# Optimization experiments

Hardware: AMD Instinct MI355X
Metric: run time of the kernel (lower is better)

Reference implementation:

```python
import jax, jax.numpy as jnp
import numpy as np

N_NODES = 100000
FEAT = 128
N_EDGES = 1600000


def setup_inputs() -> dict:
    key = jax.random.key(0)
    k1, k2, k3, k4, k5 = jax.random.split(key, 5)
    weight = jax.random.normal(k1, (N_NODES, FEAT), dtype=jnp.float32)
    cj = jax.random.uniform(k2, (N_NODES, 1), dtype=jnp.float32)
    ci = jax.random.uniform(k3, (N_NODES, 1), dtype=jnp.float32)
    src = jax.random.randint(k4, (N_EDGES,), 0, N_NODES, dtype=jnp.int32)
    dst = jax.random.randint(k5, (N_EDGES,), 0, N_NODES, dtype=jnp.int32)
    return {"weight": weight, "cj": cj, "ci": ci, "src": src, "dst": dst}


def reference(weight, cj, ci, src, dst):
    # feat = weight * dropout(cj); dropout_rate=0.0 -> identity
    feat = weight * cj                      # [N, F]
    msgs = feat[src]                        # [E, F] copy_src gather
    h = jax.ops.segment_sum(msgs, dst, num_segments=weight.shape[0])  # [N, F]
    return h * ci                           # dst-side normalize
```

## Files before the change

### kernel.cpp

```cpp
#include <hip/hip_runtime.h>
#include <hip/hip_bf16.h>

#define FEAT 128
#define BINW 128
#define BINSHIFT 7
#define MAXBIN 1024
#define MAXTILE 1024
#define FS_CAP 4096

__device__ __forceinline__ unsigned short f2b(float f) {
    __hip_bfloat16 h = __float2bfloat16(f);
    return *reinterpret_cast<unsigned short*>(&h);
}
__device__ __forceinline__ float b2f_lo(unsigned u) {
    unsigned x = u << 16;
    float f;
    __builtin_memcpy(&f, &x, 4);
    return f;
}
__device__ __forceinline__ float b2f_hi(unsigned u) {
    unsigned x = u & 0xFFFF0000u;
    float f;
    __builtin_memcpy(&f, &x, 4);
    return f;
}
__device__ __forceinline__ unsigned int pack2(float lo, float hi) {
    return (unsigned int)f2b(lo) | ((unsigned int)f2b(hi) << 16);
}


__global__ void convert_hist_bins_kernel(const float* __restrict__ weight,
                                         const float* __restrict__ cj,
                                         const int* __restrict__ dst,
                                         unsigned short* __restrict__ feat16,
                                         int* __restrict__ cnt,
                                         int N, int E, int NBIN, int tb, int ipt) {
    __shared__ int h[MAXBIN];
    int tile = blockIdx.x;
    for (int b = threadIdx.x; b < NBIN; b += 256) h[b] = 0;
    __syncthreads();

    int NC = N * (FEAT / 8);
    int cbase = tile * 256 * ipt;
    for (int j = 0; j < ipt; ++j) {
        int i = cbase + j * 256 + threadIdx.x;
        if (i < NC) {
            int row = i >> 4;
            int seg = i & 15;
            float c = cj[row];
            const float4* p = reinterpret_cast<const float4*>(
                weight + (size_t)row * FEAT + seg * 8);
            float4 a = p[0], b4 = p[1];
            uint4 o;
            o.x = pack2(a.x * c, a.y * c);
            o.y = pack2(a.z * c, a.w * c);
            o.z = pack2(b4.x * c, b4.y * c);
            o.w = pack2(b4.z * c, b4.w * c);
            *reinterpret_cast<uint4*>(feat16 + (size_t)i * 8) = o;
        }
    }

    int e0 = tile * tb;
    int iters = tb >> 8;
    for (int i = 0; i < iters; ++i) {
        int e = e0 + i * 256 + threadIdx.x;
        if (e < E) atomicAdd(&h[dst[e] >> BINSHIFT], 1);
    }
    __syncthreads();
    for (int b = threadIdx.x; b < NBIN; b += 256) cnt[(size_t)tile * NBIN + b] = h[b];
}

__global__ void bin_scan_kernel(const int* __restrict__ cnt, int* __restrict__ base_local,
                                int* __restrict__ binTot, int NBIN, int NTILE) {
    __shared__ int s[MAXTILE];
    int b = blockIdx.x;
    int t = threadIdx.x;
    int v = (t < NTILE) ? cnt[(size_t)t * NBIN + b] : 0;
    s[t] = v;
    __syncthreads();
    for (int off = 1; off < MAXTILE; off <<= 1) {
        int u = (t >= off) ? s[t - off] : 0;
        __syncthreads();
        s[t] += u;
        __syncthreads();
    }
    if (t < NTILE) base_local[(size_t)t * NBIN + b] = s[t] - v;
    if (t == MAXTILE - 1) binTot[b] = s[t];
}

__global__ void scan_tot_kernel(const int* __restrict__ binTot, int* __restrict__ binStart,
                                int NBIN) {
    __shared__ int s[1024];
    int t = threadIdx.x;
    int v = (t < NBIN) ? binTot[t] : 0;
    s[t] = v;
    __syncthreads();
    for (int off = 1; off < 1024; off <<= 1) {
        int u = (t >= off) ? s[t - off] : 0;
        __syncthreads();
        s[t] += u;
        __syncthreads();
    }
    if (t < NBIN) binStart[t] = s[t] - v;
    if (t == NBIN - 1) binStart[NBIN] = s[t];
}

__global__ void scatter_pairs_kernel(const int* __restrict__ src, const int* __restrict__ dst,
                                     const int* __restrict__ base_local,
                                     const int* __restrict__ binStart,
                                     unsigned* __restrict__ pair,
                                     int E, int NBIN, int tb) {
    __shared__ int base_l[MAXBIN];
    __shared__ int cur[MAXBIN];
    int tile = blockIdx.x;
    for (int b = threadIdx.x; b < NBIN; b += 256) {
        base_l[b] = binStart[b] + base_local[(size_t)tile * NBIN + b];
        cur[b] = 0;
    }
    __syncthreads();
    int e0 = tile * tb;
    int iters = tb >> 8;
    for (int i = 0; i < iters; ++i) {
        int e = e0 + i * 256 + threadIdx.x;
        if (e < E) {
            int d = dst[e];
            int b = d >> BINSHIFT;
            int pos = atomicAdd(&cur[b], 1);
            pair[base_l[b] + pos] = (unsigned)src[e] | ((unsigned)(d & (BINW - 1)) << 17);
        }
    }
}

__global__ void fine_sort_kernel(unsigned* __restrict__ pair,
                                 unsigned* __restrict__ tmp,
                                 const int* __restrict__ binStart,
                                 int* __restrict__ offsets,
                                 int N, int E) {
    __shared__ int cnt[BINW];
    __shared__ int sbase[BINW];
    __shared__ unsigned stage[FS_CAP];
    int bin = blockIdx.x;
    int t = threadIdx.x;
    if (t < BINW) cnt[t] = 0;
    __syncthreads();
    int start = binStart[bin];
    int end   = binStart[bin + 1];
    bool lds_ok = (end - start) <= FS_CAP;

    if (lds_ok) {
        for (int k = start + t; k < end; k += 256) {
            unsigned p = pair[k];
            stage[k - start] = p;
            atomicAdd(&cnt[p >> 17], 1);
        }
    } else {
        for (int k = start + t; k < end; k += 256) {
            unsigned p = pair[k];
            tmp[k] = p;
            atomicAdd(&cnt[p >> 17], 1);
        }
    }
    __syncthreads();
    int mine = (t < BINW) ? cnt[t] : 0;
    if (t < BINW) sbase[t] = mine;
    __syncthreads();
    for (int d = 1; d < BINW; d <<= 1) {
        int v = 0;
        if (t < BINW && t >= d) v = sbase[t - d];
        __syncthreads();
        if (t < BINW) sbase[t] += v;
        __syncthreads();
    }
    if (t < BINW) {
        int excl = sbase[t] - mine;
        int node = (bin << BINSHIFT) + t;
        if (node < N) offsets[node] = start + excl;
        sbase[t] = start + excl;
        cnt[t] = 0;
    }
    if (bin == 0 && t == 0) offsets[N] = E;
    __syncthreads();
    if (lds_ok) {
        for (int k = start + t; k < end; k += 256) {
            unsigned p = stage[k - start];
            int ld = p >> 17;
            int pos = atomicAdd(&cnt[ld], 1);
            pair[sbase[ld] + pos] = p & 0x1FFFF;
        }
    } else {
        for (int k = start + t; k < end; k += 256) {
            unsigned p = tmp[k];
            int ld = p >> 17;
            int pos = atomicAdd(&cnt[ld], 1);
            pair[sbase[ld] + pos] = p & 0x1FFFF;
        }
    }
}

__global__ void gather_kernel(const unsigned short* __restrict__ feat16,
                              const float* __restrict__ ci,
                              const int* __restrict__ offsets,
                              const int* __restrict__ src_sorted,
                              float* __restrict__ out, int N) {
    int gt = blockIdx.x * blockDim.x + threadIdx.x;
    int node = gt >> 6;
    if (node >= N) return;
    int lane = gt & 63;
    int fi   = (lane & 15) << 3;
    int q    = lane >> 4;
    int start = offsets[node];
    int end   = offsets[node + 1];
    float acc[8] = {0.f, 0.f, 0.f, 0.f, 0.f, 0.f, 0.f, 0.f};
    #pragma unroll 4
    for (int k = start + q; k < end; k += 4) {
        int s = src_sorted[k];
        uint4 u = *reinterpret_cast<const uint4*>(feat16 + ((size_t)s << 7) + fi);
        acc[0] += b2f_lo(u.x); acc[1] += b2f_hi(u.x);
        acc[2] += b2f_lo(u.y); acc[3] += b2f_hi(u.y);
        acc[4] += b2f_lo(u.z); acc[5] += b2f_hi(u.z);
        acc[6] += b2f_lo(u.w); acc[7] += b2f_hi(u.w);
    }
    #pragma unroll
    for (int j = 0; j < 8; ++j) {
        acc[j] += __shfl_xor(acc[j], 16);
        acc[j] += __shfl_xor(acc[j], 32);
    }
    if (q == 0) {
        float c = ci[node];
        float4 v0 = make_float4(acc[0] * c, acc[1] * c, acc[2] * c, acc[3] * c);
        float4 v1 = make_float4(acc[4] * c, acc[5] * c, acc[6] * c, acc[7] * c);
        float* o = out + ((size_t)node << 7) + fi;
        *reinterpret_cast<float4*>(o)     = v0;
        *reinterpret_cast<float4*>(o + 4) = v1;
    }
}


__global__ void zero_ints_kernel(int* __restrict__ p, int n) {
    int i = blockIdx.x * blockDim.x + threadIdx.x;
    if (i < n) p[i] = 0;
}

__global__ void convert_hist_kernel(const float* __restrict__ weight,
                                    const float* __restrict__ cj,
                                    const int* __restrict__ dst,
                                    int* __restrict__ counts,
                                    unsigned short* __restrict__ feat16,
                                    int N, int E) {
    int i = blockIdx.x * blockDim.x + threadIdx.x;
    int NC = N * (FEAT / 8);
    if (i < NC) {
        int row = i >> 4;
        int seg = i & 15;
        float c = cj[row];
        const float4* p = reinterpret_cast<const float4*>(weight + (size_t)row * FEAT + seg * 8);
        float4 a = p[0], b = p[1];
        uint4 o;
        o.x = pack2(a.x * c, a.y * c);
        o.y = pack2(a.z * c, a.w * c);
        o.z = pack2(b.x * c, b.y * c);
        o.w = pack2(b.z * c, b.w * c);
        *reinterpret_cast<uint4*>(feat16 + (size_t)i * 8) = o;
    }
    if (i < E) atomicAdd(&counts[dst[i]], 1);
}

__global__ void block_sum_kernel(const int* __restrict__ counts, int* __restrict__ bsum, int N) {
    __shared__ int s[256];
    int i = blockIdx.x * 256 + threadIdx.x;
    s[threadIdx.x] = (i < N) ? counts[i] : 0;
    __syncthreads();
    for (int off = 128; off > 0; off >>= 1) {
        if (threadIdx.x < off) s[threadIdx.x] += s[threadIdx.x + off];
        __syncthreads();
    }
    if (threadIdx.x == 0) bsum[blockIdx.x] = s[0];
}

__global__ void scan_bsum_kernel(int* __restrict__ bsum, int nb) {
    __shared__ int s[512];
    int t = threadIdx.x;
    int mine = (t < nb) ? bsum[t] : 0;
    s[t] = mine;
    __syncthreads();
    for (int off = 1; off < 512; off <<= 1) {
        int v = (t >= off) ? s[t - off] : 0;
        __syncthreads();
        s[t] += v;
        __syncthreads();
    }
    if (t < nb) bsum[t] = s[t] - mine;
}

__global__ void scan_counts_kernel(const int* __restrict__ counts, const int* __restrict__ bsum,
                                   int* __restrict__ offsets, int* __restrict__ cursor,
                                   int N, int E) {
    __shared__ int s[256];
    int t = threadIdx.x;
    int i = blockIdx.x * 256 + t;
    int mine = (i < N) ? counts[i] : 0;
    s[t] = mine;
    __syncthreads();
    for (int off = 1; off < 256; off <<= 1) {
        int v = (t >= off) ? s[t - off] : 0;
        __syncthreads();
        s[t] += v;
        __syncthreads();
    }
    if (i < N) {
        int o = bsum[blockIdx.x] + s[t] - mine;
        offsets[i] = o;
        cursor[i] = o;
    }
    if (i == 0 && blockIdx.x == 0) offsets[N] = E;
}

__global__ void bucket_kernel(const int* __restrict__ src, const int* __restrict__ dst,
                              int* __restrict__ cursor,
                              int* __restrict__ src_sorted, int E) {
    int i = blockIdx.x * blockDim.x + threadIdx.x;
    if (i < E) {
        int pos = atomicAdd(&cursor[dst[i]], 1);
        src_sorted[pos] = src[i];
    }
}


__global__ void gcmc_zero_kernel(float4* __restrict__ out, int n4) {
    int i = blockIdx.x * blockDim.x + threadIdx.x;
    if (i < n4) out[i] = make_float4(0.f, 0.f, 0.f, 0.f);
}

__global__ void gcmc_scatter_kernel(const float* __restrict__ weight,
                                    const float* __restrict__ cj,
                                    const int* __restrict__ src,
                                    const int* __restrict__ dst,
                                    float* __restrict__ out,
                                    int n_edges) {
    int t = blockIdx.x * blockDim.x + threadIdx.x;
    int e = t >> 5;
    int f = (t & 31) << 2;
    if (e >= n_edges) return;
    int s = src[e];
    int d = dst[e];
    float c = cj[s];
    const float4 w = *reinterpret_cast<const float4*>(weight + (size_t)s * FEAT + f);
    float* o = out + (size_t)d * FEAT + f;
    unsafeAtomicAdd(o + 0, w.x * c);
    unsafeAtomicAdd(o + 1, w.y * c);
    unsafeAtomicAdd(o + 2, w.z * c);
    unsafeAtomicAdd(o + 3, w.w * c);
}

__global__ void gcmc_scale_kernel(float4* __restrict__ out,
                                  const float* __restrict__ ci, int n4) {
    int i = blockIdx.x * blockDim.x + threadIdx.x;
    if (i < n4) {
        float c = ci[i >> 5];
        float4 v = out[i];
        v.x *= c; v.y *= c; v.z *= c; v.w *= c;
        out[i] = v;
    }
}


static inline size_t align256(size_t x) { return (x + 255) & ~(size_t)255; }

extern "C" void kernel_launch(void* const* d_in, const int* in_sizes, int n_in,
                              void* d_out, int out_size, void* d_ws, size_t ws_size,
                              hipStream_t stream) {
    const float* weight = (const float*)d_in[0];
    const float* cj     = (const float*)d_in[1];
    const float* ci     = (const float*)d_in[2];
    const int*   src    = (const int*)d_in[3];
    const int*   dst    = (const int*)d_in[4];
    float* out = (float*)d_out;

    const int N = in_sizes[1];
    const int E = in_sizes[3];

    const int NBIN = (N + BINW - 1) >> BINSHIFT;

    for (int tb = 2048; tb <= 8192; tb *= 4) {
        const int NTILE = (E + tb - 1) / tb;
        if (NTILE > MAXTILE) continue;

        size_t o_feat = 0;
        size_t o_pair = align256(o_feat + (size_t)N * FEAT * 2);
        size_t o_cnt  = align256(o_pair + (size_t)E * 4);
        size_t o_base = align256(o_cnt + (size_t)NTILE * NBIN * 4);
        size_t o_tot  = align256(o_base + (size_t)NTILE * NBIN * 4);
        size_t o_bs   = align256(o_tot + (size_t)NBIN * 4);
        size_t o_off  = align256(o_bs + (size_t)(NBIN + 1) * 4);
        size_t need   = o_off + (size_t)(N + 1) * 4;

        if (ws_size < need || NBIN > MAXBIN || N > (1 << 17) || out_size < E) continue;

        char* ws = (char*)d_ws;
        unsigned short* feat16 = (unsigned short*)(ws + o_feat);
        unsigned* pair   = (unsigned*)(ws + o_pair);
        int* cnt         = (int*)(ws + o_cnt);
        int* base_local  = (int*)(ws + o_base);
        int* binTot      = (int*)(ws + o_tot);
        int* binStart    = (int*)(ws + o_bs);
        int* offsets     = (int*)(ws + o_off);

        const int NC  = N * (FEAT / 8);
        const int ipt = (NC + NTILE * 256 - 1) / (NTILE * 256);

        convert_hist_bins_kernel<<<NTILE, 256, 0, stream>>>(
            weight, cj, dst, feat16, cnt, N, E, NBIN, tb, ipt);
        bin_scan_kernel<<<NBIN, MAXTILE, 0, stream>>>(cnt, base_local, binTot, NBIN, NTILE);
        scan_tot_kernel<<<1, 1024, 0, stream>>>(binTot, binStart, NBIN);
        scatter_pairs_kernel<<<NTILE, 256, 0, stream>>>(src, dst, base_local, binStart,
                                                        pair, E, NBIN, tb);
        fine_sort_kernel<<<NBIN, 256, 0, stream>>>(pair, (unsigned*)out, binStart,
                                                   offsets, N, E);
        long threads = (long)N * 64;
        gather_kernel<<<(int)((threads + 255) / 256), 256, 0, stream>>>(
            feat16, ci, offsets, (const int*)pair, out, N);
        return;
    }

    const int NB = (N + 255) / 256;
    size_t m_off = 0;
    size_t m_cur = align256(m_off + (size_t)(N + 1) * 4);
    size_t m_bsm = align256(m_cur + (size_t)N * 4);
    size_t m_src = align256(m_bsm + 512 * 4);
    size_t m_ft  = align256(m_src + (size_t)E * 4);
    size_t need_mid = m_ft + (size_t)N * FEAT * 2;

    if (ws_size >= need_mid && NB <= 512) {
        char* ws = (char*)d_ws;
        int* offsets    = (int*)(ws + m_off);
        int* cursor     = (int*)(ws + m_cur);
        int* bsum       = (int*)(ws + m_bsm);
        int* src_sorted = (int*)(ws + m_src);
        unsigned short* feat16 = (unsigned short*)(ws + m_ft);

        zero_ints_kernel<<<NB, 256, 0, stream>>>(cursor, N);
        {
            long T = (long)N * (FEAT / 8);
            if ((long)E > T) T = E;
            convert_hist_kernel<<<(int)((T + 255) / 256), 256, 0, stream>>>(
                weight, cj, dst, cursor, feat16, N, E);
        }
        block_sum_kernel<<<NB, 256, 0, stream>>>(cursor, bsum, N);
        scan_bsum_kernel<<<1, 512, 0, stream>>>(bsum, NB);
        scan_counts_kernel<<<NB, 256, 0, stream>>>(cursor, bsum, offsets, cursor, N, E);
        bucket_kernel<<<(E + 255) / 256, 256, 0, stream>>>(src, dst, cursor, src_sorted, E);
        long threads = (long)N * 64;
        gather_kernel<<<(int)((threads + 255) / 256), 256, 0, stream>>>(
            feat16, ci, offsets, src_sorted, out, N);
        return;
    }

    const int total = N * FEAT;
    const int n4 = total >> 2;
    gcmc_zero_kernel<<<(n4 + 255) / 256, 256, 0, stream>>>((float4*)out, n4);
    const long threads = (long)E * 32;
    gcmc_scatter_kernel<<<(int)((threads + 255) / 256), 256, 0, stream>>>(
        weight, cj, src, dst, out, E);
    gcmc_scale_kernel<<<(n4 + 255) / 256, 256, 0, stream>>>((float4*)out, ci, n4);
}
```

Measured before the change: 131.4 us.

## Fuse fine sort into gather and assign bin starts atomically

Merges the per-bin fine sort with the gather so each block sorts its bin's edges in LDS and aggregates features directly, so sorted edges and offsets no longer round-trip through global memory. The bin-total scan kernel is dropped: bin starts come from an atomic cursor instead of a prefix scan. Bins shrink to 64 nodes, tile count is capped at 256, and the convert grid is doubled so conversion is spread across more blocks. Bins larger than the LDS capacity are handled by chunking, with read-modify-write of the output; the atomic ordering makes bin layout nondeterministic and the gather now runs with fewer, larger blocks.

After: 143.6 us. 9.3% more time.

```diff
diff --git a/kernel.cpp b/kernel.cpp
--- a/kernel.cpp
+++ b/kernel.cpp
@@ -2,11 +2,11 @@
 #include <hip/hip_bf16.h>
 
 #define FEAT 128
-#define BINW 128
-#define BINSHIFT 7
-#define MAXBIN 1024
-#define MAXTILE 1024
-#define FS_CAP 4096
+#define BINW 64
+#define BINSHIFT 6
+#define MAXBIN 2048
+#define MAXTILE 256
+#define FS_CAP 2048
 
 __device__ __forceinline__ unsigned short f2b(float f) {
     __hip_bfloat16 h = __float2bfloat16(f);
@@ -34,11 +34,12 @@
                                          const int* __restrict__ dst,
                                          unsigned short* __restrict__ feat16,
                                          int* __restrict__ cnt,
-                                         int N, int E, int NBIN, int tb, int ipt) {
+                                         int* __restrict__ cursor,
+                                         int N, int E, int NBIN, int NTILE,
+                                         int tb, int ipt) {
     __shared__ int h[MAXBIN];
     int tile = blockIdx.x;
-    for (int b = threadIdx.x; b < NBIN; b += 256) h[b] = 0;
-    __syncthreads();
+    if (tile == 0 && threadIdx.x == 0) *cursor = 0;
 
     int NC = N * (FEAT / 8);
     int cbase = tile * 256 * ipt;
@@ -60,18 +61,27 @@
         }
     }
 
-    int e0 = tile * tb;
-    int iters = tb >> 8;
-    for (int i = 0; i < iters; ++i) {
-        int e = e0 + i * 256 + threadIdx.x;
-        if (e < E) atomicAdd(&h[dst[e] >> BINSHIFT], 1);
-    }
-    __syncthreads();
-    for (int b = threadIdx.x; b < NBIN; b += 256) cnt[(size_t)tile * NBIN + b] = h[b];
-}
-
-__global__ void bin_scan_kernel(const int* __restrict__ cnt, int* __restrict__ base_local,
-                                int* __restrict__ binTot, int NBIN, int NTILE) {
+    if (tile < NTILE) {
+        for (int b = threadIdx.x; b < NBIN; b += 256) h[b] = 0;
+        __syncthreads();
+        int e0 = tile * tb;
+        int iters = tb >> 8;
+        for (int i = 0; i < iters; ++i) {
+            int e = e0 + i * 256 + threadIdx.x;
+            if (e < E) atomicAdd(&h[dst[e] >> BINSHIFT], 1);
+        }
+        __syncthreads();
+        for (int b = threadIdx.x; b < NBIN; b += 256)
+            cnt[(size_t)tile * NBIN + b] = h[b];
+    }
+}
+
+__global__ void bin_scan_kernel(const int* __restrict__ cnt,
+                                int* __restrict__ base_local,
+                                int* __restrict__ binStart,
+                                int* __restrict__ binLen,
+                                int* __restrict__ cursor,
+                                int NBIN, int NTILE) {
     __shared__ int s[MAXTILE];
     int b = blockIdx.x;
     int t = threadIdx.x;
@@ -85,24 +95,11 @@
         __syncthreads();
     }
     if (t < NTILE) base_local[(size_t)t * NBIN + b] = s[t] - v;
-    if (t == MAXTILE - 1) binTot[b] = s[t];
-}
-
-__global__ void scan_tot_kernel(const int* __restrict__ binTot, int* __restrict__ binStart,
-                                int NBIN) {
-    __shared__ int s[1024];
-    int t = threadIdx.x;
-    int v = (t < NBIN) ? binTot[t] : 0;
-    s[t] = v;
-    __syncthreads();
-    for (int off = 1; off < 1024; off <<= 1) {
-        int u = (t >= off) ? s[t - off] : 0;
-        __syncthreads();
-        s[t] += u;
-        __syncthreads();
-    }
-    if (t < NBIN) binStart[t] = s[t] - v;
-    if (t == NBIN - 1) binStart[NBIN] = s[t];
+    if (t == MAXTILE - 1) {
+        int tot = s[t];
+        binLen[b] = tot;
+        binStart[b] = atomicAdd(cursor, tot);
+    }
 }
 
 __global__ void scatter_pairs_kernel(const int* __restrict__ src, const int* __restrict__ dst,
@@ -131,69 +128,198 @@
     }
 }
 
-__global__ void fine_sort_kernel(unsigned* __restrict__ pair,
-                                 unsigned* __restrict__ tmp,
-                                 const int* __restrict__ binStart,
-                                 int* __restrict__ offsets,
-                                 int N, int E) {
+__global__ void __launch_bounds__(512)
+gather_sort_kernel(const unsigned short* __restrict__ feat16,
+                   const float* __restrict__ ci,
+                   const int* __restrict__ binStart,
+                   const int* __restrict__ binLen,
+                   const unsigned* __restrict__ pair,
+                   float* __restrict__ out, int N) {
+    __shared__ unsigned stage[FS_CAP];
+    __shared__ int srt[FS_CAP];
     __shared__ int cnt[BINW];
     __shared__ int sbase[BINW];
-    __shared__ unsigned stage[FS_CAP];
+
     int bin = blockIdx.x;
     int t = threadIdx.x;
-    if (t < BINW) cnt[t] = 0;
-    __syncthreads();
     int start = binStart[bin];
-    int end   = binStart[bin + 1];
-    bool lds_ok = (end - start) <= FS_CAP;
-
-    if (lds_ok) {
-        for (int k = start + t; k < end; k += 256) {
-            unsigned p = pair[k];
-            stage[k - start] = p;
+    int len   = binLen[bin];
+    int w    = t >> 6;
+    int lane = t & 63;
+    int q    = lane >> 4;
+    int fi   = (lane & 15) << 3;
+
+    int nchunks = (len + FS_CAP - 1) / FS_CAP;
+    if (nchunks < 1) nchunks = 1;
+
+    for (int ic = 0; ic < nchunks; ++ic) {
+        __syncthreads();
+        int cs = start + ic * FS_CAP;
+        int clen = len - ic * FS_CAP;
+        if (clen > FS_CAP) clen = FS_CAP;
+        if (clen < 0) clen = 0;
+
+        if (t < BINW) cnt[t] = 0;
+        __syncthreads();
+        for (int k = t; k < clen; k += 512) {
+            unsigned p = pair[cs + k];
+            stage[k] = p;
             atomicAdd(&cnt[p >> 17], 1);
         }
-    } else {
-        for (int k = start + t; k < end; k += 256) {
-            unsigned p = pair[k];
-            tmp[k] = p;
-            atomicAdd(&cnt[p >> 17], 1);
-        }
-    }
-    __syncthreads();
-    int mine = (t < BINW) ? cnt[t] : 0;
-    if (t < BINW) sbase[t] = mine;
-    __syncthreads();
-    for (int d = 1; d < BINW; d <<= 1) {
-        int v = 0;
-        if (t < BINW && t >= d) v = sbase[t - d];
-        __syncthreads();
-        if (t < BINW) sbase[t] += v;
-        __syncthreads();
-    }
-    if (t < BINW) {
-        int excl = sbase[t] - mine;
-        int node = (bin << BINSHIFT) + t;
-        if (node < N) offsets[node] = start + excl;
-        sbase[t] = start + excl;
-        cnt[t] = 0;
-    }
-    if (bin == 0 && t == 0) offsets[N] = E;
-    __syncthreads();
-    if (lds_ok) {
-        for (int k = start + t; k < end; k += 256) {
-            unsigned p = stage[k - start];
+        __syncthreads();
+        int mine = (t < BINW) ? cnt[t] : 0;
+        if (t < BINW) sbase[t] = mine;
+        __syncthreads();
+        for (int d = 1; d < BINW; d <<= 1) {
+            int v = 0;
+            if (t < BINW && t >= d) v = sbase[t - d];
+            __syncthreads();
+            if (t < BINW) sbase[t] += v;
+            __syncthreads();
+        }
+        if (t < BINW) { sbase[t] -= mine; cnt[t] = 0; }
+        __syncthreads();
+        for (int k = t; k < clen; k += 512) {
+            unsigned p = stage[k];
             int ld = p >> 17;
             int pos = atomicAdd(&cnt[ld], 1);
-            pair[sbase[ld] + pos] = p & 0x1FFFF;
-        }
-    } else {
-        for (int k = start + t; k < end; k += 256) {
-            unsigned p = tmp[k];
-            int ld = p >> 17;
-            int pos = atomicAdd(&cnt[ld], 1);
-            pair[sbase[ld] + pos] = p & 0x1FFFF;
-        }
+            srt[sbase[ld] + pos] = (int)(p & 0x1FFFF);
+        }
+        __syncthreads();
+
+        bool first = (ic == 0);
+        bool last  = (ic == nchunks - 1);
+        for (int j = 0; j < 8; ++j) {
+            int ln = (w << 3) + j;
+            int node = (bin << BINSHIFT) + ln;
+            if (node >= N) break;
+            int sb = sbase[ln];
+            int c  = cnt[ln];
+            float acc[8] = {0.f, 0.f, 0.f, 0.f, 0.f, 0.f, 0.f, 0.f};
+            #pragma unroll 4
+            for (int k = q; k < c; k += 4) {
+                int s = srt[sb + k];
+                uint4 u = *reinterpret_cast<const uint4*>(
+                    feat16 + ((size_t)s << 7) + fi);
+                acc[0] += b2f_lo(u.x); acc[1] += b2f_hi(u.x);
+                acc[2] += b2f_lo(u.y); acc[3] += b2f_hi(u.y);
+                acc[4] += b2f_lo(u.z); acc[5] += b2f_hi(u.z);
+                acc[6] += b2f_lo(u.w); acc[7] += b2f_hi(u.w);
+            }
+            #pragma unroll
+            for (int r = 0; r < 8; ++r) {
+                acc[r] += __shfl_xor(acc[r], 16);
+                acc[r] += __shfl_xor(acc[r], 32);
+            }
+            if (q == 0) {
+                float* o = out + ((size_t)node << 7) + fi;
+                float4 v0 = make_float4(acc[0], acc[1], acc[2], acc[3]);
+                float4 v1 = make_float4(acc[4], acc[5], acc[6], acc[7]);
+                if (!first) {
+                    float4 p0 = *reinterpret_cast<float4*>(o);
+                    float4 p1 = *reinterpret_cast<float4*>(o + 4);
+                    v0.x += p0.x; v0.y += p0.y; v0.z += p0.z; v0.w += p0.w;
+                    v1.x += p1.x; v1.y += p1.y; v1.z += p1.z; v1.w += p1.w;
+                }
+                if (last) {
+                    float cc = ci[node];
+                    v0.x *= cc; v0.y *= cc; v0.z *= cc; v0.w *= cc;
+                    v1.x *= cc; v1.y *= cc; v1.z *= cc; v1.w *= cc;
+                }
+                *reinterpret_cast<float4*>(o)     = v0;
+                *reinterpret_cast<float4*>(o + 4) = v1;
+            }
+        }
+    }
+}
+
+
+__global__ void zero_ints_kernel(int* __restrict__ p, int n) {
+    int i = blockIdx.x * blockDim.x + threadIdx.x;
+    if (i < n) p[i] = 0;
+}
+
+__global__ void convert_hist_kernel(const float* __restrict__ weight,
+                                    const float* __restrict__ cj,
+                                    const int* __restrict__ dst,
+                                    int* __restrict__ counts,
+                                    unsigned short* __restrict__ feat16,
+                                    int N, int E) {
+    int i = blockIdx.x * blockDim.x + threadIdx.x;
+    int NC = N * (FEAT / 8);
+    if (i < NC) {
+        int row = i >> 4;
+        int seg = i & 15;
+        float c = cj[row];
+        const float4* p = reinterpret_cast<const float4*>(weight + (size_t)row * FEAT + seg * 8);
+        float4 a = p[0], b = p[1];
+        uint4 o;
+        o.x = pack2(a.x * c, a.y * c);
+        o.y = pack2(a.z * c, a.w * c);
+        o.z = pack2(b.x * c, b.y * c);
+        o.w = pack2(b.z * c, b.w * c);
+        *reinterpret_cast<uint4*>(feat16 + (size_t)i * 8) = o;
+    }
+    if (i < E) atomicAdd(&counts[dst[i]], 1);
+}
+
+__global__ void block_sum_kernel(const int* __restrict__ counts, int* __restrict__ bsum, int N) {
+    __shared__ int s[256];
+    int i = blockIdx.x * 256 + threadIdx.x;
+    s[threadIdx.x] = (i < N) ? counts[i] : 0;
+    __syncthreads();
+    for (int off = 128; off > 0; off >>= 1) {
+        if (threadIdx.x < off) s[threadIdx.x] += s[threadIdx.x + off];
+        __syncthreads();
+    }
+    if (threadIdx.x == 0) bsum[blockIdx.x] = s[0];
+}
+
+__global__ void scan_bsum_kernel(int* __restrict__ bsum, int nb) {
+    __shared__ int s[512];
+    int t = threadIdx.x;
+    int mine = (t < nb) ? bsum[t] : 0;
+    s[t] = mine;
+    __syncthreads();
+    for (int off = 1; off < 512; off <<= 1) {
+        int v = (t >= off) ? s[t - off] : 0;
+        __syncthreads();
+        s[t] += v;
+        __syncthreads();
+    }
+    if (t < nb) bsum[t] = s[t] - mine;
+}
+
+__global__ void scan_counts_kernel(const int* __restrict__ counts, const int* __restrict__ bsum,
+                                   int* __restrict__ offsets, int* __restrict__ cursor,
+                                   int N, int E) {
+    __shared__ int s[256];
+    int t = threadIdx.x;
+    int i = blockIdx.x * 256 + t;
+    int mine = (i < N) ? counts[i] : 0;
+    s[t] = mine;
+    __syncthreads();
+    for (int off = 1; off < 256; off <<= 1) {
+        int v = (t >= off) ? s[t - off] : 0;
+        __syncthreads();
+        s[t] += v;
+        __syncthreads();
+    }
+    if (i < N) {
+        int o = bsum[blockIdx.x] + s[t] - mine;
+        offsets[i] = o;
+        cursor[i] = o;
+    }
+    if (i == 0 && blockIdx.x == 0) offsets[N] = E;
+}
+
+__global__ void bucket_kernel(const int* __restrict__ src, const int* __restrict__ dst,
+                              int* __restrict__ cursor,
+                              int* __restrict__ src_sorted, int E) {
+    int i = blockIdx.x * blockDim.x + threadIdx.x;
+    if (i < E) {
+        int pos = atomicAdd(&cursor[dst[i]], 1);
+        src_sorted[pos] = src[i];
     }
 }
 
@@ -236,96 +362,6 @@
 }
 
 
-__global__ void zero_ints_kernel(int* __restrict__ p, int n) {
-    int i = blockIdx.x * blockDim.x + threadIdx.x;
-    if (i < n) p[i] = 0;
-}
-
-__global__ void convert_hist_kernel(const float* __restrict__ weight,
-                                    const float* __restrict__ cj,
-                                    const int* __restrict__ dst,
-                                    int* __restrict__ counts,
-                                    unsigned short* __restrict__ feat16,
-                                    int N, int E) {
-    int i = blockIdx.x * blockDim.x + threadIdx.x;
-    int NC = N * (FEAT / 8);
-    if (i < NC) {
-        int row = i >> 4;
-        int seg = i & 15;
-        float c = cj[row];
-        const float4* p = reinterpret_cast<const float4*>(weight + (size_t)row * FEAT + seg * 8);
-        float4 a = p[0], b = p[1];
-        uint4 o;
-        o.x = pack2(a.x * c, a.y * c);
-        o.y = pack2(a.z * c, a.w * c);
-        o.z = pack2(b.x * c, b.y * c);
-        o.w = pack2(b.z * c, b.w * c);
-        *reinterpret_cast<uint4*>(feat16 + (size_t)i * 8) = o;
-    }
-    if (i < E) atomicAdd(&counts[dst[i]], 1);
-}
-
-__global__ void block_sum_kernel(const int* __restrict__ counts, int* __restrict__ bsum, int N) {
-    __shared__ int s[256];
-    int i = blockIdx.x * 256 + threadIdx.x;
-    s[threadIdx.x] = (i < N) ? counts[i] : 0;
-    __syncthreads();
-    for (int off = 128; off > 0; off >>= 1) {
-        if (threadIdx.x < off) s[threadIdx.x] += s[threadIdx.x + off];
-        __syncthreads();
-    }
-    if (threadIdx.x == 0) bsum[blockIdx.x] = s[0];
-}
-
-__global__ void scan_bsum_kernel(int* __restrict__ bsum, int nb) {
-    __shared__ int s[512];
-    int t = threadIdx.x;
-    int mine = (t < nb) ? bsum[t] : 0;
-    s[t] = mine;
-    __syncthreads();
-    for (int off = 1; off < 512; off <<= 1) {
-        int v = (t >= off) ? s[t - off] : 0;
-        __syncthreads();
-        s[t] += v;
-        __syncthreads();
-    }
-    if (t < nb) bsum[t] = s[t] - mine;
-}
-
-__global__ void scan_counts_kernel(const int* __restrict__ counts, const int* __restrict__ bsum,
-                                   int* __restrict__ offsets, int* __restrict__ cursor,
-                                   int N, int E) {
-    __shared__ int s[256];
-    int t = threadIdx.x;
-    int i = blockIdx.x * 256 + t;
-    int mine = (i < N) ? counts[i] : 0;
-    s[t] = mine;
-    __syncthreads();
-    for (int off = 1; off < 256; off <<= 1) {
-        int v = (t >= off) ? s[t - off] : 0;
-        __syncthreads();
-        s[t] += v;
-        __syncthreads();
-    }
-    if (i < N) {
-        int o = bsum[blockIdx.x] + s[t] - mine;
-        offsets[i] = o;
-        cursor[i] = o;
-    }
-    if (i == 0 && blockIdx.x == 0) offsets[N] = E;
-}
-
-__global__ void bucket_kernel(const int* __restrict__ src, const int* __restrict__ dst,
-                              int* __restrict__ cursor,
-                              int* __restrict__ src_sorted, int E) {
-    int i = blockIdx.x * blockDim.x + threadIdx.x;
-    if (i < E) {
-        int pos = atomicAdd(&cursor[dst[i]], 1);
-        src_sorted[pos] = src[i];
-    }
-}
-
-
 __global__ void gcmc_zero_kernel(float4* __restrict__ out, int n4) {
     int i = blockIdx.x * blockDim.x + threadIdx.x;
     if (i < n4) out[i] = make_float4(0.f, 0.f, 0.f, 0.f);
@@ -381,44 +417,41 @@
 
     const int NBIN = (N + BINW - 1) >> BINSHIFT;
 
-    for (int tb = 2048; tb <= 8192; tb *= 4) {
-        const int NTILE = (E + tb - 1) / tb;
-        if (NTILE > MAXTILE) continue;
-
-        size_t o_feat = 0;
-        size_t o_pair = align256(o_feat + (size_t)N * FEAT * 2);
-        size_t o_cnt  = align256(o_pair + (size_t)E * 4);
-        size_t o_base = align256(o_cnt + (size_t)NTILE * NBIN * 4);
-        size_t o_tot  = align256(o_base + (size_t)NTILE * NBIN * 4);
-        size_t o_bs   = align256(o_tot + (size_t)NBIN * 4);
-        size_t o_off  = align256(o_bs + (size_t)(NBIN + 1) * 4);
-        size_t need   = o_off + (size_t)(N + 1) * 4;
-
-        if (ws_size < need || NBIN > MAXBIN || N > (1 << 17) || out_size < E) continue;
-
+    int tb = 8192;
+    while ((E + tb - 1) / tb > MAXTILE) tb <<= 1;
+    const int NTILE = (E + tb - 1) / tb;
+
+    size_t o_feat = 0;
+    size_t o_pair = align256(o_feat + (size_t)N * FEAT * 2);
+    size_t o_cnt  = align256(o_pair + (size_t)E * 4);
+    size_t o_base = align256(o_cnt + (size_t)NTILE * NBIN * 4);
+    size_t o_bs   = align256(o_base + (size_t)NTILE * NBIN * 4);
+    size_t o_bl   = align256(o_bs + (size_t)NBIN * 4);
+    size_t o_cur  = align256(o_bl + (size_t)NBIN * 4);
+    size_t need_new = o_cur + 256;
+
+    if (ws_size >= need_new && NBIN <= MAXBIN && NTILE <= MAXTILE && N <= (1 << 17)) {
         char* ws = (char*)d_ws;
         unsigned short* feat16 = (unsigned short*)(ws + o_feat);
         unsigned* pair   = (unsigned*)(ws + o_pair);
         int* cnt         = (int*)(ws + o_cnt);
         int* base_local  = (int*)(ws + o_base);
-        int* binTot      = (int*)(ws + o_tot);
         int* binStart    = (int*)(ws + o_bs);
-        int* offsets     = (int*)(ws + o_off);
+        int* binLen      = (int*)(ws + o_bl);
+        int* cursor      = (int*)(ws + o_cur);
 
         const int NC  = N * (FEAT / 8);
-        const int ipt = (NC + NTILE * 256 - 1) / (NTILE * 256);
-
-        convert_hist_bins_kernel<<<NTILE, 256, 0, stream>>>(
-            weight, cj, dst, feat16, cnt, N, E, NBIN, tb, ipt);
-        bin_scan_kernel<<<NBIN, MAXTILE, 0, stream>>>(cnt, base_local, binTot, NBIN, NTILE);
-        scan_tot_kernel<<<1, 1024, 0, stream>>>(binTot, binStart, NBIN);
-        scatter_pairs_kernel<<<NTILE, 256, 0, stream>>>(src, dst, base_local, binStart,
-                                                        pair, E, NBIN, tb);
-        fine_sort_kernel<<<NBIN, 256, 0, stream>>>(pair, (unsigned*)out, binStart,
-                                                   offsets, N, E);
-        long threads = (long)N * 64;
-        gather_kernel<<<(int)((threads + 255) / 256), 256, 0, stream>>>(
-            feat16, ci, offsets, (const int*)pair, out, N);
+        const int G   = 2 * NTILE;
+        const int ipt = (NC + G * 256 - 1) / (G * 256);
+
+        convert_hist_bins_kernel<<<G, 256, 0, stream>>>(
+            weight, cj, dst, feat16, cnt, cursor, N, E, NBIN, NTILE, tb, ipt);
+        bin_scan_kernel<<<NBIN, MAXTILE, 0, stream>>>(
+            cnt, base_local, binStart, binLen, cursor, NBIN, NTILE);
+        scatter_pairs_kernel<<<NTILE, 256, 0, stream>>>(
+            src, dst, base_local, binStart, pair, E, NBIN, tb);
+        gather_sort_kernel<<<NBIN, 512, 0, stream>>>(
+            feat16, ci, binStart, binLen, pair, out, N);
         return;
     }
 
```
